# Kernel tuning notes

Measured on AMD Instinct MI355X. Metric: run time of the kernel, lower is better.

Reference implementation:

```python
import jax, jax.numpy as jnp
import numpy as np

# Module hyperparameters (init_kwargs)
KH, KW = 1, 1            # kernel_size
PATCH_H, PATCH_W = 21, 21  # patch_size (displacement grid)
SH, SW = 1, 1            # stride
PAD_H, PAD_W = 0, 0      # padding
DILP_H, DILP_W = 1, 1    # dilation_patch
B, C, H, W = 8, 256, 64, 96


def setup_inputs() -> dict:
    key = jax.random.key(0)
    k1, k2 = jax.random.split(key)
    input1 = jax.random.normal(k1, (B, C, H, W), dtype=jnp.float32)
    input2 = jax.random.normal(k2, (B, C, H, W), dtype=jnp.float32)
    return {"input1": input1, "input2": input2}


def _correlation(x1, x2):
    """FlowNet-style spatial correlation (cost volume).

    out[b, pi, pj, i, j] = sum_{c, ki, kj}
        x1_pad[b, c, i*SH + ki, j*SW + kj] *
        x2_pad[b, c, i*SH + ki + (pi - radH)*DILP_H, j*SW + kj + (pj - radW)*DILP_W]
    Out-of-bounds reads of x2 are zero (handled by padding).
    """
    radH, radW = PATCH_H // 2, PATCH_W // 2
    x1p = jnp.pad(x1, ((0, 0), (0, 0), (PAD_H, PAD_H), (PAD_W, PAD_W)))
    x2p = jnp.pad(x2, ((0, 0), (0, 0),
                       (PAD_H + radH * DILP_H, PAD_H + radH * DILP_H),
                       (PAD_W + radW * DILP_W, PAD_W + radW * DILP_W)))
    Hp, Wp = H + 2 * PAD_H, W + 2 * PAD_W
    oH = (Hp - KH) // SH + 1
    oW = (Wp - KW) // SW + 1

    # displacement grid -> start offsets into x2p (0 corresponds to -rad shift)
    sh = jnp.arange(PATCH_H, dtype=jnp.int32) * DILP_H
    sw = jnp.arange(PATCH_W, dtype=jnp.int32) * DILP_W
    starts = jnp.stack(jnp.meshgrid(sh, sw, indexing="ij"), axis=-1).reshape(-1, 2)

    def step(carry, s):
        # shifted view of x2 aligned with padded x1
        sl = jax.lax.dynamic_slice(x2p, (0, 0, s[0], s[1]), (B, C, Hp, Wp))
        prod = jnp.sum(x1p * sl, axis=1)  # [B, Hp, Wp], channel reduction
        # kernel-window sum + output stride (KH=KW=1 -> single strided slice)
        acc = jnp.zeros((B, oH, oW), dtype=prod.dtype)
        for ki in range(KH):
            for kj in range(KW):
                acc = acc + jax.lax.slice(
                    prod, (0, ki, kj),
                    (B, ki + (oH - 1) * SH + 1, kj + (oW - 1) * SW + 1),
                    (1, SH, SW))
        return carry, acc

    _, out = jax.lax.scan(step, None, starts)  # [PATCH_H*PATCH_W, B, oH, oW]
    out = out.reshape(PATCH_H, PATCH_W, B, oH, oW)
    return jnp.transpose(out, (2, 0, 1, 3, 4))  # [B, patchH, patchW, oH, oW]


def reference(input1, input2):
    return _correlation(input1, input2)
```

## Files before the change

### kernel.cpp

```cpp
#include <hip/hip_runtime.h>

typedef __attribute__((ext_vector_type(8))) short short8;
typedef __attribute__((ext_vector_type(4))) float f32x4;
typedef __attribute__((ext_vector_type(4))) unsigned short us4;

constexpr int NB = 8, NC = 256, IH = 64, IW = 96;
constexpr int PATCH = 21, RAD = 10;
constexpr int TI = 8, TJ = 8;
constexpr int WIN = 28, NWIN = 784;
constexpr int KC = 32, NKS = NC / KC;
constexpr int PLANE = IH * IW;
constexpr int PH = IH + 2 * RAD, PW = IW + 2 * RAD;
constexpr int NBCH = NWIN * 4;
constexpr int NCHUNK = NBCH + 256;
constexpr int ASTR = IH * IW * KC;
constexpr int BSTR = PH * PW * KC;
constexpr size_t X1T_ELEMS = (size_t)NB * NKS * ASTR;
constexpr size_t X2P_ELEMS = (size_t)NB * NKS * BSTR;
constexpr int GSTR = 65;
constexpr int X1BLKS = NB * IH * 8;
constexpr int X2BLKS = NB * PH * 8;

__device__ __forceinline__ unsigned short f2bf(float f) {
  unsigned u = __builtin_bit_cast(unsigned, f);
  u += 0x7fffu + ((u >> 16) & 1u);
  return (unsigned short)(u >> 16);
}

__global__ __launch_bounds__(256) void prepass_kmajor(
    const float* __restrict__ x1, const float* __restrict__ x2,
    unsigned short* __restrict__ x1k, unsigned short* __restrict__ x2k) {
  __shared__ float lsf[32 * 97];
  const int t = threadIdx.x;
  if (blockIdx.x < X1BLKS) {
    const int blk = blockIdx.x;
    const int ct = blk & 7, i = (blk >> 3) & 63, b = blk >> 9;
    const int c0 = ct * 32;
    const float* sp = x1 + ((size_t)b * NC + c0) * PLANE + (size_t)i * IW;
#pragma unroll
    for (int k = 0; k < 3; ++k) {
      int idx = k * 256 + t;
      int c = idx / 24, j4 = idx - c * 24;
      f32x4 v = *(const f32x4*)(sp + (size_t)c * PLANE + 4 * j4);
      float* lp = &lsf[c * 97 + 4 * j4];
      lp[0] = v[0]; lp[1] = v[1]; lp[2] = v[2]; lp[3] = v[3];
    }
    __syncthreads();
    unsigned short* dp = x1k + (((size_t)(b * NKS + ct) * IH + i) * IW) * KC;
#pragma unroll
    for (int k = 0; k < 3; ++k) {
      int o = k * 256 + t;
      int j = o >> 3, cq = o & 7;
      us4 v = {f2bf(lsf[(cq * 4 + 0) * 97 + j]), f2bf(lsf[(cq * 4 + 1) * 97 + j]),
               f2bf(lsf[(cq * 4 + 2) * 97 + j]), f2bf(lsf[(cq * 4 + 3) * 97 + j])};
      *(us4*)&dp[(size_t)j * KC + cq * 4] = v;
    }
  } else {
    const int blk = blockIdx.x - X1BLKS;
    const int ct = blk & 7, i = (blk >> 3) % PH, b = blk / (PH * 8);
    const int c0 = ct * 32;
    const int isrc = i - RAD;
    const bool rowok = (unsigned)isrc < (unsigned)IH;
    if (rowok) {
      const float* sp = x2 + ((size_t)b * NC + c0) * PLANE + (size_t)isrc * IW;
#pragma unroll
      for (int k = 0; k < 3; ++k) {
        int idx = k * 256 + t;
        int c = idx / 24, j4 = idx - c * 24;
        f32x4 v = *(const f32x4*)(sp + (size_t)c * PLANE + 4 * j4);
        float* lp = &lsf[c * 97 + 4 * j4];
        lp[0] = v[0]; lp[1] = v[1]; lp[2] = v[2]; lp[3] = v[3];
      }
    }
    __syncthreads();
    unsigned short* dp = x2k + (((size_t)(b * NKS + ct) * PH + i) * PW) * KC;
#pragma unroll
    for (int k = 0; k < 4; ++k) {
      int o = k * 256 + t;
      if (o < PW * 8) {
        int j = o >> 3, cq = o & 7;
        int jsrc = j - RAD;
        us4 v = {0, 0, 0, 0};
        if (rowok && (unsigned)jsrc < (unsigned)IW)
          v = us4{f2bf(lsf[(cq * 4 + 0) * 97 + jsrc]), f2bf(lsf[(cq * 4 + 1) * 97 + jsrc]),
                  f2bf(lsf[(cq * 4 + 2) * 97 + jsrc]), f2bf(lsf[(cq * 4 + 3) * 97 + jsrc])};
        *(us4*)&dp[(size_t)j * KC + cq * 4] = v;
      }
    }
  }
}

__global__ __launch_bounds__(512, 2) void corr_pipe8(
    const unsigned short* __restrict__ x1k, const unsigned short* __restrict__ x2k,
    float* __restrict__ out) {
  __shared__ __attribute__((aligned(16))) unsigned short ls[3 * NCHUNK * 8];

  const int t = threadIdx.x, lane = t & 63, wv = t >> 6;
  const int bid = blockIdx.x;
  const int b = bid & 7;
  const int tile = bid >> 3;
  const int ti = tile / 12, tj = tile - ti * 12;
  const int i0 = ti * TI, j0 = tj * TJ;
  const int cbeg = 6 * wv;
  const int qk = lane >> 4, lr = lane & 15;

  const unsigned short* x1b = x1k + (size_t)b * NKS * ASTR;
  const unsigned short* x2b = x2k + (size_t)b * NKS * BSTR;

  const unsigned short* srcp[7];
#pragma unroll
  for (int it = 0; it < 7; ++it) {
    int q = it * 512 + t;
    if (q < NBCH) {
      int w = ((q >> 3) << 1) | (((q >> 2) ^ (q >> 4)) & 1);
      int c4 = (q & 3) ^ (w & 3);
      int wi = w / WIN, wj = w - wi * WIN;
      srcp[it] = x2b + ((size_t)(i0 + wi) * PW + (j0 + wj)) * KC + c4 * 8;
    } else {
      int qa = (q - NBCH) & 255;
      int m = ((qa >> 3) << 1) | (((qa >> 2) ^ (qa >> 4)) & 1);
      int c4 = (qa & 3) ^ (m & 3);
      srcp[it] = x1b + ((size_t)(i0 + (m >> 3)) * IW + (j0 + (m & 7))) * KC + c4 * 8;
    }
  }

  f32x4 acc[4][7];
#pragma unroll
  for (int a = 0; a < 4; ++a)
#pragma unroll
    for (int cc = 0; cc < 7; ++cc) acc[a][cc] = (f32x4){0.f, 0.f, 0.f, 0.f};

#define STAGE(BUF, KS)                                                              \
  {                                                                                 \
    unsigned short* lb = &ls[(BUF) * NCHUNK * 8];                                   \
    _Pragma("unroll")                                                               \
    for (int it = 0; it < 6; ++it)                                                  \
      __builtin_amdgcn_global_load_lds(                                             \
          (const void*)(srcp[it] + (size_t)(KS) * BSTR),                            \
          (void*)(lb + (it * 512 + wv * 64) * 8), 16, 0, 0);                        \
    if (wv < 5)                                                                     \
      __builtin_amdgcn_global_load_lds(                                             \
          (const void*)(srcp[6] + (size_t)(KS) * (wv == 0 ? BSTR : ASTR)),          \
          (void*)(lb + (3072 + wv * 64) * 8), 16, 0, 0);                            \
  }

#define COMPUTE(BUF)                                                                \
  {                                                                                 \
    const unsigned short* lb = &ls[(BUF) * NCHUNK * 8];                             \
    short8 af0 = *(const short8*)(lb + (NBCH + ((4 * (lr) + qk) ^ (lr & 7))) * 8);        \
    short8 af1 = *(const short8*)(lb + (NBCH + ((4 * (16 + lr) + qk) ^ (lr & 7))) * 8);   \
    short8 af2 = *(const short8*)(lb + (NBCH + ((4 * (32 + lr) + qk) ^ (lr & 7))) * 8);   \
    short8 af3 = *(const short8*)(lb + (NBCH + ((4 * (48 + lr) + qk) ^ (lr & 7))) * 8);   \
    _Pragma("unroll")                                                               \
    for (int cc = 0; cc < 7; ++cc) {                                                \
      int wrow = 16 * (cbeg + cc) + lr;                                             \
      int slot = (4 * wrow + qk) ^ (lr & 7);                                        \
      short8 bf = *(const short8*)(lb + slot * 8);                                  \
      acc[0][cc] = __builtin_amdgcn_mfma_f32_16x16x32_bf16(af0, bf, acc[0][cc], 0, 0, 0); \
      acc[1][cc] = __builtin_amdgcn_mfma_f32_16x16x32_bf16(af1, bf, acc[1][cc], 0, 0, 0); \
      acc[2][cc] = __builtin_amdgcn_mfma_f32_16x16x32_bf16(af2, bf, acc[2][cc], 0, 0, 0); \
      acc[3][cc] = __builtin_amdgcn_mfma_f32_16x16x32_bf16(af3, bf, acc[3][cc], 0, 0, 0); \
    }                                                                               \
  }

  STAGE(0, 0)
  STAGE(1, 1)

#define ITER(KS, VM)                                           \
  if ((KS) < 6) STAGE(((KS) + 2) % 3, (KS) + 2)                \
  asm volatile("s_waitcnt vmcnt(" #VM ")" ::: "memory");       \
  asm volatile("s_barrier" ::: "memory");                      \
  COMPUTE((KS) % 3)                                            \
  asm volatile("s_barrier" ::: "memory");

  ITER(0, 12)
  ITER(1, 12)
  ITER(2, 12)
  ITER(3, 12)
  ITER(4, 12)
  ITER(5, 12)
  ITER(6, 6)
  ITER(7, 0)
#undef ITER
#undef COMPUTE
#undef STAGE

  float* gf = (float*)ls;
#pragma unroll
  for (int ch = 0; ch < 2; ++ch) {
    __syncthreads();
    const int n0 = ch ? 384 : 0;
#pragma unroll
    for (int a = 0; a < 4; ++a)
#pragma unroll
      for (int cc = 0; cc < 7; ++cc) {
        int ccg = cbeg + cc;
        if (ch ? (ccg >= 24) : (ccg <= 24)) {
          int nl = 16 * ccg + lr - n0;
          int mb = 16 * a + 4 * qk;
          float* gp = &gf[nl * GSTR + mb];
          gp[0] = acc[a][cc][0]; gp[1] = acc[a][cc][1];
          gp[2] = acc[a][cc][2]; gp[3] = acc[a][cc][3];
        }
      }
    __syncthreads();
    for (int s = t; s < 1764; s += 512) {
      int pidx = s / 21, pj = s - pidx * 21;
      int ii = 0, rem = pidx, stop = 0;
#pragma unroll
      for (int k = 0; k < 7; ++k) {
        int cnt = ch ? (7 + k) : (14 - k);
        int go = (!stop) && (rem >= cnt);
        rem -= go ? cnt : 0;
        ii += go;
        stop |= !go;
      }
      int pi = ch ? (14 - ii + rem) : rem;
      int nl = 28 * (pi + ii) + pj - n0;
      int ms = 8 * ii;
      float g[8];
#pragma unroll
      for (int e = 0; e < 8; ++e) g[e] = gf[(nl + e) * GSTR + ms + e];
      float* op = out + ((((size_t)b * PATCH + pi) * PATCH + pj) * IH + (i0 + ii)) * IW + j0;
      f32x4 v0 = {g[0], g[1], g[2], g[3]};
      f32x4 v1 = {g[4], g[5], g[6], g[7]};
      *(f32x4*)op = v0;
      *(f32x4*)(op + 4) = v1;
    }
  }
}

constexpr int LDKF = 40;
__global__ __launch_bounds__(512, 2) void corr_mfma_fb(
    const float* __restrict__ x1, const float* __restrict__ x2, float* __restrict__ out) {
  __shared__ __attribute__((aligned(16))) unsigned short lsA[64 * LDKF];
  __shared__ __attribute__((aligned(16))) unsigned short lsB[NWIN * LDKF];
  const int t = threadIdx.x;
  const int b = blockIdx.y;
  const int ti = blockIdx.x / 12, tj = blockIdx.x % 12;
  const int i0 = ti * TI, j0 = tj * TJ;
  const int lane = t & 63, wv = t >> 6;
  const int mtp = wv >> 2, cg = wv & 3, cbeg = cg * 12;
  const int qk = lane >> 4, lr = lane & 15;
  f32x4 acc[2][13];
#pragma unroll
  for (int a = 0; a < 2; ++a)
#pragma unroll
    for (int cc = 0; cc < 13; ++cc) acc[a][cc] = (f32x4){0.f, 0.f, 0.f, 0.f};
  const int am = t & 63, ak4 = t >> 6;
  const int aii = am >> 3, ajj = am & 7;
  const float* x1p = x1 + ((size_t)b * NC + 4 * ak4) * PLANE + (size_t)(i0 + aii) * IW + (j0 + ajj);
  const float* x2b = x2 + (size_t)b * NC * PLANE;
  for (int ks = 0; ks < NKS; ++ks) {
    __syncthreads();
    {
      const float* p = x1p + (size_t)ks * KC * PLANE;
      us4 v = {f2bf(p[0]), f2bf(p[PLANE]), f2bf(p[2 * PLANE]), f2bf(p[3 * PLANE])};
      *(us4*)&lsA[am * LDKF + 4 * ak4] = v;
    }
    for (int w = t; w < NWIN; w += 512) {
      const int wi = w / WIN, wj = w - wi * WIN;
      const int gi = i0 - RAD + wi, gj = j0 - RAD + wj;
      const bool ok = ((unsigned)gi < (unsigned)IH) && ((unsigned)gj < (unsigned)IW);
      const float* p = x2b + ((size_t)(ks * KC) * IH + gi) * IW + gj;
      unsigned short* dst = &lsB[w * LDKF];
#pragma unroll
      for (int k4 = 0; k4 < 8; ++k4) {
        const float* q = p + (size_t)(4 * k4) * PLANE;
        us4 v = {f2bf(ok ? q[0] : 0.f), f2bf(ok ? q[PLANE] : 0.f),
                 f2bf(ok ? q[2 * PLANE] : 0.f), f2bf(ok ? q[3 * PLANE] : 0.f)};
        *(us4*)&dst[4 * k4] = v;
      }
    }
    __syncthreads();
    short8 a0 = *(const short8*)&lsA[(32 * mtp + lr) * LDKF + 8 * qk];
    short8 a1 = *(const short8*)&lsA[(32 * mtp + 16 + lr) * LDKF + 8 * qk];
#pragma unroll
    for (int cc = 0; cc < 13; ++cc) {
      const int wrow = 16 * (cbeg + cc) + lr;
      short8 bf = *(const short8*)&lsB[wrow * LDKF + 8 * qk];
      acc[0][cc] = __builtin_amdgcn_mfma_f32_16x16x32_bf16(a0, bf, acc[0][cc], 0, 0, 0);
      acc[1][cc] = __builtin_amdgcn_mfma_f32_16x16x32_bf16(a1, bf, acc[1][cc], 0, 0, 0);
    }
  }
#pragma unroll
  for (int a = 0; a < 2; ++a) {
    const int mb = 16 * (2 * mtp + a) + qk * 4;
#pragma unroll
    for (int cc = 0; cc < 13; ++cc) {
      if (cg > 0 && cc == 0) continue;
      const int n = 16 * (cbeg + cc) + lr;
      const int wi = n / WIN, wj = n - wi * WIN;
#pragma unroll
      for (int r = 0; r < 4; ++r) {
        const int m = mb + r;
        const int ii = m >> 3, jj = m & 7;
        const int pi = wi - ii, pj = wj - jj;
        if ((unsigned)pi < (unsigned)PATCH && (unsigned)pj < (unsigned)PATCH)
          out[((((size_t)b * PATCH + pi) * PATCH + pj) * IH + (i0 + ii)) * IW + (j0 + jj)] =
              acc[a][cc][r];
      }
    }
  }
}

extern "C" void kernel_launch(void* const* d_in, const int* in_sizes, int n_in,
                              void* d_out, int out_size, void* d_ws, size_t ws_size,
                              hipStream_t stream) {
  const float* x1 = (const float*)d_in[0];
  const float* x2 = (const float*)d_in[1];
  float* out = (float*)d_out;
  const size_t need = (X1T_ELEMS + X2P_ELEMS) * sizeof(unsigned short);
  if (ws_size >= need) {
    unsigned short* x1k = (unsigned short*)d_ws;
    unsigned short* x2k = x1k + X1T_ELEMS;
    prepass_kmajor<<<X1BLKS + X2BLKS, 256, 0, stream>>>(x1, x2, x1k, x2k);
    corr_pipe8<<<NB * 96, 512, 0, stream>>>(x1k, x2k, out);
  } else {
    dim3 grid(96, NB);
    corr_mfma_fb<<<grid, 512, 0, stream>>>(x1, x2, out);
  }
}
```

Baseline: 84.62 us.

## Give each wave a private LDS window pipeline and load A into registers

```diff
diff --git a/kernel.cpp b/kernel.cpp
--- a/kernel.cpp
+++ b/kernel.cpp
@@ -11,8 +11,8 @@
 constexpr int KC = 32, NKS = NC / KC;
 constexpr int PLANE = IH * IW;
 constexpr int PH = IH + 2 * RAD, PW = IW + 2 * RAD;
-constexpr int NBCH = NWIN * 4;
-constexpr int NCHUNK = NBCH + 256;
+constexpr int WCH = 448;
+constexpr int WBUF = 8 * WCH;
 constexpr int ASTR = IH * IW * KC;
 constexpr int BSTR = PH * PW * KC;
 constexpr size_t X1T_ELEMS = (size_t)NB * NKS * ASTR;
@@ -90,10 +90,10 @@
   }
 }
 
-__global__ __launch_bounds__(512, 2) void corr_pipe8(
+__global__ __launch_bounds__(512, 2) void corr_wavepipe(
     const unsigned short* __restrict__ x1k, const unsigned short* __restrict__ x2k,
     float* __restrict__ out) {
-  __shared__ __attribute__((aligned(16))) unsigned short ls[3 * NCHUNK * 8];
+  __shared__ __attribute__((aligned(16))) unsigned short ls[2 * WBUF * 8];
 
   const int t = threadIdx.x, lane = t & 63, wv = t >> 6;
   const int bid = blockIdx.x;
@@ -109,20 +109,17 @@
 
   const unsigned short* srcp[7];
 #pragma unroll
-  for (int it = 0; it < 7; ++it) {
-    int q = it * 512 + t;
-    if (q < NBCH) {
-      int w = ((q >> 3) << 1) | (((q >> 2) ^ (q >> 4)) & 1);
-      int c4 = (q & 3) ^ (w & 3);
-      int wi = w / WIN, wj = w - wi * WIN;
-      srcp[it] = x2b + ((size_t)(i0 + wi) * PW + (j0 + wj)) * KC + c4 * 8;
-    } else {
-      int qa = (q - NBCH) & 255;
-      int m = ((qa >> 3) << 1) | (((qa >> 2) ^ (qa >> 4)) & 1);
-      int c4 = (qa & 3) ^ (m & 3);
-      srcp[it] = x1b + ((size_t)(i0 + (m >> 3)) * IW + (j0 + (m & 7))) * KC + c4 * 8;
-    }
-  }
+  for (int s = 0; s < 7; ++s) {
+    int c = s * 64 + lane;
+    int w = ((c >> 3) << 1) | (((c >> 2) ^ (c >> 4)) & 1);
+    int c4 = (c & 3) ^ (w & 3);
+    int n = 96 * wv + w;
+    int wi = n / WIN, wj = n - wi * WIN;
+    srcp[s] = x2b + ((size_t)(i0 + wi) * PW + (j0 + wj)) * KC + c4 * 8;
+  }
+  const unsigned short* srcA =
+      x1b + ((size_t)(i0 + (lr >> 3)) * IW + (j0 + (lr & 7))) * KC + qk * 8;
+  constexpr size_t AOFF = (size_t)2 * IW * KC;
 
   f32x4 acc[4][7];
 #pragma unroll
@@ -130,60 +127,65 @@
 #pragma unroll
     for (int cc = 0; cc < 7; ++cc) acc[a][cc] = (f32x4){0.f, 0.f, 0.f, 0.f};
 
-#define STAGE(BUF, KS)                                                              \
+  short8 aA0, aA1, aA2, aA3, aB0, aB1, aB2, aB3;
+
+#define ALOAD(S, KS)                                                                \
   {                                                                                 \
-    unsigned short* lb = &ls[(BUF) * NCHUNK * 8];                                   \
+    const unsigned short* ap = srcA + (size_t)(KS) * ASTR;                          \
+    a##S##0 = *(const short8*)(ap);                                                 \
+    a##S##1 = *(const short8*)(ap + AOFF);                                          \
+    a##S##2 = *(const short8*)(ap + 2 * AOFF);                                      \
+    a##S##3 = *(const short8*)(ap + 3 * AOFF);                                      \
+  }
+
+#define STAGEW(BUF, KS)                                                             \
+  {                                                                                 \
+    unsigned short* lb = &ls[((BUF) * WBUF + wv * WCH) * 8];                        \
     _Pragma("unroll")                                                               \
-    for (int it = 0; it < 6; ++it)                                                  \
+    for (int s = 0; s < 7; ++s)                                                     \
       __builtin_amdgcn_global_load_lds(                                             \
-          (const void*)(srcp[it] + (size_t)(KS) * BSTR),                            \
-          (void*)(lb + (it * 512 + wv * 64) * 8), 16, 0, 0);                        \
-    if (wv < 5)                                                                     \
-      __builtin_amdgcn_global_load_lds(                                             \
-          (const void*)(srcp[6] + (size_t)(KS) * (wv == 0 ? BSTR : ASTR)),          \
-          (void*)(lb + (3072 + wv * 64) * 8), 16, 0, 0);                            \
-  }
-
-#define COMPUTE(BUF)                                                                \
+          (const void*)(srcp[s] + (size_t)(KS) * BSTR),                             \
+          (void*)(lb + s * 512), 16, 0, 0);                                         \
+  }
+
+#define COMPUTE(BUF, S)                                                             \
   {                                                                                 \
-    const unsigned short* lb = &ls[(BUF) * NCHUNK * 8];                             \
-    short8 af0 = *(const short8*)(lb + (NBCH + ((4 * (lr) + qk) ^ (lr & 7))) * 8);        \
-    short8 af1 = *(const short8*)(lb + (NBCH + ((4 * (16 + lr) + qk) ^ (lr & 7))) * 8);   \
-    short8 af2 = *(const short8*)(lb + (NBCH + ((4 * (32 + lr) + qk) ^ (lr & 7))) * 8);   \
-    short8 af3 = *(const short8*)(lb + (NBCH + ((4 * (48 + lr) + qk) ^ (lr & 7))) * 8);   \
+    const unsigned short* lb = &ls[((BUF) * WBUF + wv * WCH) * 8];                  \
     _Pragma("unroll")                                                               \
     for (int cc = 0; cc < 7; ++cc) {                                                \
-      int wrow = 16 * (cbeg + cc) + lr;                                             \
-      int slot = (4 * wrow + qk) ^ (lr & 7);                                        \
+      int wl = 16 * cc + lr;                                                        \
+      int slot = (4 * wl + qk) ^ (lr & 7);                                          \
       short8 bf = *(const short8*)(lb + slot * 8);                                  \
-      acc[0][cc] = __builtin_amdgcn_mfma_f32_16x16x32_bf16(af0, bf, acc[0][cc], 0, 0, 0); \
-      acc[1][cc] = __builtin_amdgcn_mfma_f32_16x16x32_bf16(af1, bf, acc[1][cc], 0, 0, 0); \
-      acc[2][cc] = __builtin_amdgcn_mfma_f32_16x16x32_bf16(af2, bf, acc[2][cc], 0, 0, 0); \
-      acc[3][cc] = __builtin_amdgcn_mfma_f32_16x16x32_bf16(af3, bf, acc[3][cc], 0, 0, 0); \
+      acc[0][cc] = __builtin_amdgcn_mfma_f32_16x16x32_bf16(a##S##0, bf, acc[0][cc], 0, 0, 0); \
+      acc[1][cc] = __builtin_amdgcn_mfma_f32_16x16x32_bf16(a##S##1, bf, acc[1][cc], 0, 0, 0); \
+      acc[2][cc] = __builtin_amdgcn_mfma_f32_16x16x32_bf16(a##S##2, bf, acc[2][cc], 0, 0, 0); \
+      acc[3][cc] = __builtin_amdgcn_mfma_f32_16x16x32_bf16(a##S##3, bf, acc[3][cc], 0, 0, 0); \
     }                                                                               \
   }
 
-  STAGE(0, 0)
-  STAGE(1, 1)
-
-#define ITER(KS, VM)                                           \
-  if ((KS) < 6) STAGE(((KS) + 2) % 3, (KS) + 2)                \
-  asm volatile("s_waitcnt vmcnt(" #VM ")" ::: "memory");       \
-  asm volatile("s_barrier" ::: "memory");                      \
-  COMPUTE((KS) % 3)                                            \
-  asm volatile("s_barrier" ::: "memory");
-
-  ITER(0, 12)
-  ITER(1, 12)
-  ITER(2, 12)
-  ITER(3, 12)
-  ITER(4, 12)
-  ITER(5, 12)
-  ITER(6, 6)
-  ITER(7, 0)
+  ALOAD(A, 0)
+  STAGEW(0, 0)
+  asm volatile("" ::: "memory");
+  ALOAD(B, 1)
+  STAGEW(1, 1)
+
+#define ITER(KS, SL, SC, VM)                                                        \
+  if ((KS) >= 1 && (KS) < 7) { ALOAD(SL, (KS) + 1) STAGEW(((KS) + 1) & 1, (KS) + 1) } \
+  asm volatile("s_waitcnt vmcnt(" #VM ")" ::: "memory");                            \
+  COMPUTE((KS) & 1, SC)
+
+  ITER(0, A, A, 11)
+  ITER(1, A, B, 11)
+  ITER(2, B, A, 11)
+  ITER(3, A, B, 11)
+  ITER(4, B, A, 11)
+  ITER(5, A, B, 11)
+  ITER(6, B, A, 11)
+  ITER(7, A, B, 0)
 #undef ITER
 #undef COMPUTE
-#undef STAGE
+#undef STAGEW
+#undef ALOAD
 
   float* gf = (float*)ls;
 #pragma unroll
@@ -315,7 +317,7 @@
     unsigned short* x1k = (unsigned short*)d_ws;
     unsigned short* x2k = x1k + X1T_ELEMS;
     prepass_kmajor<<<X1BLKS + X2BLKS, 256, 0, stream>>>(x1, x2, x1k, x2k);
-    corr_pipe8<<<NB * 96, 512, 0, stream>>>(x1k, x2k, out);
+    corr_wavepipe<<<NB * 96, 512, 0, stream>>>(x1k, x2k, out);
   } else {
     dim3 grid(96, NB);
     corr_mfma_fb<<<grid, 512, 0, stream>>>(x1, x2, out);
```

After: 85.64 us. Within noise of the previous version (+1.2%).
